# Kernel tuning notes

Hardware: AMD Instinct MI355X
Metric: run time of the kernel (lower is better)

Reference implementation:

```python
import jax, jax.numpy as jnp
import numpy as np
import math

D_MODEL = 1024
MEM_SIZE = 4096
N_HEADS = 8
BATCH = 4
SEQ = 1024
TOP_K = min(SEQ, MEM_SIZE // 10)  # 409, matches torch: min(seq_len, memory_size//10)
UPDATE_RATE = 0.01


def _gelu(x):
    return jax.nn.gelu(x, approximate=False)  # torch nn.GELU default (erf)


def setup_inputs() -> dict:
    key = jax.random.key(0)
    ks = jax.random.split(key, 26)
    w = lambda k, shape, s=0.02: (jax.random.normal(k, shape, jnp.float32) * s)
    inp = {
        "x": jax.random.normal(ks[0], (BATCH, SEQ, D_MODEL), jnp.float32),
        "memory_bank": jax.random.normal(ks[1], (MEM_SIZE, D_MODEL), jnp.float32) * 0.1,
        "memory_indices": jax.random.randint(ks[2], (BATCH, TOP_K), 0, MEM_SIZE, jnp.int32),
        # memory_encoder: Linear -> GELU -> Linear
        "enc_w1": w(ks[3], (D_MODEL, D_MODEL)), "enc_b1": jnp.zeros((D_MODEL,), jnp.float32),
        "enc_w2": w(ks[4], (D_MODEL, D_MODEL)), "enc_b2": jnp.zeros((D_MODEL,), jnp.float32),
        # MultiheadAttention in/out projections
        "wq": w(ks[5], (D_MODEL, D_MODEL)), "bq": jnp.zeros((D_MODEL,), jnp.float32),
        "wk": w(ks[6], (D_MODEL, D_MODEL)), "bk": jnp.zeros((D_MODEL,), jnp.float32),
        "wv": w(ks[7], (D_MODEL, D_MODEL)), "bv": jnp.zeros((D_MODEL,), jnp.float32),
        "wo": w(ks[8], (D_MODEL, D_MODEL)), "bo": jnp.zeros((D_MODEL,), jnp.float32),
        # memory_decoder: Linear -> GELU -> Linear
        "dec_w1": w(ks[9], (D_MODEL, D_MODEL)), "dec_b1": jnp.zeros((D_MODEL,), jnp.float32),
        "dec_w2": w(ks[10], (D_MODEL, D_MODEL)), "dec_b2": jnp.zeros((D_MODEL,), jnp.float32),
        # LayerNorm
        "ln_g": jnp.ones((D_MODEL,), jnp.float32), "ln_b": jnp.zeros((D_MODEL,), jnp.float32),
        # importance_scorer: Linear(d,64) -> GELU -> Linear(64,1) -> Sigmoid
        "imp_w1": w(ks[11], (D_MODEL, 64)), "imp_b1": jnp.zeros((64,), jnp.float32),
        "imp_w2": w(ks[12], (64, 1)), "imp_b2": jnp.zeros((1,), jnp.float32),
    }
    return inp


def reference(x, memory_bank, memory_indices,
              enc_w1, enc_b1, enc_w2, enc_b2,
              wq, bq, wk, bk, wv, bv, wo, bo,
              dec_w1, dec_b1, dec_w2, dec_b2,
              ln_g, ln_b, imp_w1, imp_b1, imp_w2, imp_b2):
    B, L, D = x.shape
    M = memory_bank.shape[0]
    H = N_HEADS
    dh = D // H

    # memory_encoder (dropout inactive at eval)
    enc = _gelu(x @ enc_w1 + enc_b1) @ enc_w2 + enc_b2  # [B,L,D]

    # cross-attention: query = encoded input, key/value = memory bank (shared across batch)
    q = (enc @ wq + bq).reshape(B, L, H, dh)
    k = (memory_bank @ wk + bk).reshape(M, H, dh)
    v = (memory_bank @ wv + bv).reshape(M, H, dh)
    scores = jnp.einsum('blhd,mhd->bhlm', q, k) * (1.0 / math.sqrt(dh))
    attn = jax.nn.softmax(scores, axis=-1)                 # [B,H,L,M]
    ctx = jnp.einsum('bhlm,mhd->blhd', attn, v).reshape(B, L, D)
    mem_out = ctx @ wo + bo

    # memory_decoder + residual + LayerNorm
    dec = _gelu(mem_out @ dec_w1 + dec_b1) @ dec_w2 + dec_b2
    comb = x + dec
    mu = jnp.mean(comb, axis=-1, keepdims=True)
    var = jnp.var(comb, axis=-1, keepdims=True)
    out = (comb - mu) / jnp.sqrt(var + 1e-5) * ln_g + ln_b  # [B,L,D]

    # _update_memory: importance top-k select + sequential EMA scatter into memory bank
    imp = jax.nn.sigmoid(_gelu(x @ imp_w1 + imp_b1) @ imp_w2 + imp_b2)[..., 0]  # [B,L]
    _, top_idx = jax.lax.top_k(imp, TOP_K)                  # [B,K]
    top_tok = jnp.take_along_axis(x, top_idx[..., None], axis=1)  # [B,K,D]

    # faithful to the torch double loop (b outer, k inner): sequential EMA with
    # chained updates on index collisions
    flat_idx = memory_indices.reshape(-1)
    flat_tok = top_tok.reshape(-1, D)

    def body(mem, xs):
        i, t = xs
        row = (1.0 - UPDATE_RATE) * mem[i] + UPDATE_RATE * t
        return mem.at[i].set(row), None

    new_mem, _ = jax.lax.scan(body, memory_bank, (flat_idx, flat_tok))
    return out, new_mem
```

## Files before the change

### kernel.cpp

```cpp
#include <hip/hip_runtime.h>

typedef unsigned short u16;
typedef __attribute__((ext_vector_type(4))) int i4;
typedef __attribute__((ext_vector_type(4))) unsigned u4;
typedef __attribute__((ext_vector_type(4))) unsigned short us4;
typedef __attribute__((ext_vector_type(8))) short short8;
typedef __attribute__((ext_vector_type(4))) float f4;

#define D_MODEL 1024
#define ROWS 4096
#define NHEAD 8
#define DH 128
#define TOPK 409
#define NUPD 1636
#define NBATCH 4
#define MAXC 64
#define ATTNROWS 32768

__device__ __forceinline__ u16 f2bf(float f) {
  unsigned u = __builtin_bit_cast(unsigned, f);
  u += 0x7fffu + ((u >> 16) & 1u);
  return (u16)(u >> 16);
}
__device__ __forceinline__ float bf2f(u16 b) {
  unsigned u = ((unsigned)b) << 16;
  return __builtin_bit_cast(float, u);
}
__device__ __forceinline__ float gelu_f(float v) {
  return 0.5f * v * (1.0f + erff(v * 0.70710678118654752f));
}
__device__ __forceinline__ void gload16(const void* g, void* l) {
  __builtin_amdgcn_global_load_lds((const __attribute__((address_space(1))) void*)g,
                                   (__attribute__((address_space(3))) void*)l, 16, 0, 0);
}

__global__ __launch_bounds__(256) void conv2_kernel(const float* __restrict__ in0,
                                                    u16* __restrict__ out0,
                                                    const float* __restrict__ in1,
                                                    u16* __restrict__ out1, int nb) {
  int bid = blockIdx.x;
  const float* in = (bid < nb) ? in0 : in1;
  u16* out = (bid < nb) ? out0 : out1;
  int i = (bid < nb ? bid : bid - nb) * 256 + threadIdx.x;
  f4 v = ((const f4*)in)[i];
  us4 o;
  o.x = f2bf(v.x); o.y = f2bf(v.y); o.z = f2bf(v.z); o.w = f2bf(v.w);
  ((us4*)out)[i] = o;
}

__global__ __launch_bounds__(256) void wtrans8_kernel(const float* s0, const float* s1,
                                                      const float* s2, const float* s3,
                                                      const float* s4, const float* s5,
                                                      const float* s6, const float* s7,
                                                      u16* __restrict__ dst) {
  const float* srcs[8] = {s0, s1, s2, s3, s4, s5, s6, s7};
  const float* w = srcs[blockIdx.z];
  u16* wt = dst + (size_t)blockIdx.z * (1024 * 1024);
  __shared__ float t[32][33];
  int tx = threadIdx.x & 31, ty = threadIdx.x >> 5;
  int k0 = blockIdx.y * 32, n0 = blockIdx.x * 32;
  for (int r = 0; r < 4; ++r)
    t[ty + r * 8][tx] = w[(size_t)(k0 + ty + r * 8) * 1024 + n0 + tx];
  __syncthreads();
  for (int r = 0; r < 4; ++r)
    wt[(size_t)(n0 + ty + r * 8) * 1024 + k0 + tx] = f2bf(t[tx][ty + r * 8]);
}

__global__ __launch_bounds__(256) void bias_partB(const float* __restrict__ pbuf,
                                                  const float* __restrict__ bq,
                                                  const float* __restrict__ db1,
                                                  float* __restrict__ bqp,
                                                  float* __restrict__ bodp) {
  int id = blockIdx.x;
  int which = id >> 2;
  int n = (id & 3) * 256 + threadIdx.x;
  float s = 0.0f;
  for (int kb = 0; kb < 8; ++kb) s += pbuf[(size_t)(which * 8 + kb) * 1024 + n];
  float* out = which ? bodp : bqp;
  const float* badd = which ? db1 : bq;
  out[n] = s + badd[n];
}

__device__ __forceinline__ void gemm_core(const u16* __restrict__ A,
                                          const u16* __restrict__ BT,
                                          char* al, char* bl, int m0, int n0,
                                          f4 acc[4][2]) {
  const int K = 1024;
  const int tid = threadIdx.x;
  const int lane = tid & 63;
  const int g = lane >> 4, qi = lane & 15;
  const int wid = tid >> 6;
  const int wr = wid >> 1, wc = wid & 1;
  const int a0r = tid >> 2, a0b = (tid & 3) ^ ((a0r >> 1) & 3);
  const int c1 = tid + 256;
  const int a1r = c1 >> 2, a1b = (c1 & 3) ^ ((a1r >> 1) & 3);
  const int b0r = tid >> 2, b0b = (tid & 3) ^ ((b0r >> 1) & 3);

#define STAGE(buf, kt)                                                                   \
  {                                                                                      \
    const int k0_ = (kt) * 32;                                                           \
    gload16(A + (size_t)(m0 + a0r) * K + k0_ + a0b * 8, al + (buf) * 8192 + tid * 16);   \
    gload16(A + (size_t)(m0 + a1r) * K + k0_ + a1b * 8, al + (buf) * 8192 + c1 * 16);    \
    gload16(BT + (size_t)(n0 + b0r) * K + k0_ + b0b * 8, bl + (buf) * 4096 + tid * 16);  \
  }

  STAGE(0, 0);
  __syncthreads();
  int cur = 0;
  for (int kt = 0; kt < 32; ++kt) {
    if (kt + 1 < 32) STAGE(cur ^ 1, kt + 1);
    short8 af[4], bfr[2];
    for (int i = 0; i < 4; ++i) {
      int r = wr * 64 + i * 16 + qi;
      af[i] = *(const short8*)(al + cur * 8192 + r * 64 + ((g ^ ((r >> 1) & 3))) * 16);
    }
    for (int sn = 0; sn < 2; ++sn) {
      int r = wc * 32 + sn * 16 + qi;
      bfr[sn] = *(const short8*)(bl + cur * 4096 + r * 64 + ((g ^ ((r >> 1) & 3))) * 16);
    }
    for (int i = 0; i < 4; ++i)
      for (int sn = 0; sn < 2; ++sn)
        acc[i][sn] = __builtin_amdgcn_mfma_f32_16x16x32_bf16(af[i], bfr[sn], acc[i][sn], 0, 0, 0);
    __syncthreads();
    cur ^= 1;
  }
#undef STAGE
}

__global__ __launch_bounds__(256) void mega_kernel(
    const u16* __restrict__ Akv, const u16* __restrict__ BTkv,
    const float* __restrict__ bk, const float* __restrict__ bv,
    u16* __restrict__ Ck, u16* __restrict__ CvT,
    const u16* __restrict__ Ae, const u16* __restrict__ BTe,
    const float* __restrict__ be, u16* __restrict__ Ce,
    const u16* __restrict__ A0, const u16* __restrict__ B0, u16* __restrict__ C0,
    const u16* __restrict__ A1, const u16* __restrict__ B1, u16* __restrict__ C1,
    const float* __restrict__ b2, const float* __restrict__ wqf,
    const float* __restrict__ bo, const float* __restrict__ dw1,
    float* __restrict__ pbuf) {
  __shared__ __align__(16) char pool[2 * 128 * 64 + 2 * 64 * 64];
  char* al = pool;
  char* bl = pool + 2 * 128 * 64;
  const int gid = blockIdx.x;
  const int tid = threadIdx.x;
  const int lane = tid & 63, wid = tid >> 6;
  const int g = lane >> 4, qi = lane & 15;
  const int wr = wid >> 1, wc = wid & 1;

  if (gid < 1024) {
    const int xcd = gid & 7, j = gid >> 3;
    const int m0 = ((j & 3) * 8 + xcd) * 128;
    const int n0 = (j >> 2) * 64;
    f4 acc[4][2] = {};
    gemm_core(Akv, BTkv, al, bl, m0, n0, acc);
    if (n0 < 1024) {
      for (int i = 0; i < 4; ++i) {
        int row = m0 + wr * 64 + i * 16 + g * 4;
        for (int sn = 0; sn < 2; ++sn) {
          int col = n0 + wc * 32 + sn * 16 + qi;
          float bvv = bk[col];
          for (int jj = 0; jj < 4; ++jj)
            Ck[(size_t)(row + jj) * 1024 + col] = f2bf(acc[i][sn][jj] + bvv);
        }
      }
    } else {
      u16(*t)[132] = (u16(*)[132])pool;
      __syncthreads();
      for (int i = 0; i < 4; ++i)
        for (int sn = 0; sn < 2; ++sn) {
          int nl = wc * 32 + sn * 16 + qi;
          float bvv = bv[n0 - 1024 + nl];
          for (int jj = 0; jj < 4; ++jj)
            t[nl][wr * 64 + i * 16 + g * 4 + jj] = f2bf(acc[i][sn][jj] + bvv);
        }
      __syncthreads();
      int r = tid >> 2, cg = tid & 3;
      for (int v = 0; v < 4; ++v) {
        us4 val = *(const us4*)&t[r][cg * 32 + v * 8];
        *(us4*)&CvT[(size_t)(n0 - 1024 + r) * 4096 + m0 + cg * 32 + v * 8] = val;
      }
    }
  } else if (gid < 1536) {
    const int id = gid - 1024;
    const int xcd = id & 7, j = id >> 3;
    const int m0 = ((j & 3) * 8 + xcd) * 128;
    const int n0 = (j >> 2) * 64;
    f4 acc[4][2] = {};
    gemm_core(Ae, BTe, al, bl, m0, n0, acc);
    for (int i = 0; i < 4; ++i) {
      int row = m0 + wr * 64 + i * 16 + g * 4;
      for (int sn = 0; sn < 2; ++sn) {
        int col = n0 + wc * 32 + sn * 16 + qi;
        float bv = be[col];
        for (int jj = 0; jj < 4; ++jj)
          Ce[(size_t)(row + jj) * 1024 + col] = f2bf(gelu_f(acc[i][sn][jj] + bv));
      }
    }
  } else if (gid < 1792) {
    const int id = gid - 1536;
    const int which = id >> 7, j = id & 127;
    const u16* A = which ? A1 : A0;
    const u16* BT = which ? B1 : B0;
    u16* C = which ? C1 : C0;
    const int m0 = (j >> 4) * 128, n0 = (j & 15) * 64;
    f4 acc[4][2] = {};
    gemm_core(A, BT, al, bl, m0, n0, acc);
    for (int i = 0; i < 4; ++i) {
      int row = m0 + wr * 64 + i * 16 + g * 4;
      for (int sn = 0; sn < 2; ++sn) {
        int col = n0 + wc * 32 + sn * 16 + qi;
        for (int jj = 0; jj < 4; ++jj)
          C[(size_t)(row + jj) * 1024 + col] = f2bf(acc[i][sn][jj]);
      }
    }
  } else {
    const int lid = gid - 1792;
    const int which = lid >> 5;
    const int kb = (lid >> 2) & 7;
    const int n = (lid & 3) * 256 + tid;
    const float* bvec = which ? bo : b2;
    const float* W = which ? dw1 : wqf;
    float s = 0.0f;
    for (int k = kb * 128; k < kb * 128 + 128; ++k) s += bvec[k] * W[(size_t)k * 1024 + n];
    pbuf[(size_t)(which * 8 + kb) * 1024 + n] = s;
  }
}

template <int EPI>
__global__ __launch_bounds__(256) void gemm_bt(const u16* __restrict__ A,
                                               const u16* __restrict__ BT,
                                               const float* __restrict__ bias,
                                               void* __restrict__ C) {
  __shared__ __align__(16) char al[2 * 128 * 64];
  __shared__ __align__(16) char bl[2 * 64 * 64];
  const int N = 1024;
  const int id = blockIdx.x;
  const int xcd = id & 7, j = id >> 3;
  const int m0 = ((j & 3) * 8 + xcd) * 128;
  const int n0 = (j >> 2) * 64;
  const int tid = threadIdx.x;
  const int lane = tid & 63, wid = tid >> 6;
  const int g = lane >> 4, qi = lane & 15;
  const int wr = wid >> 1, wc = wid & 1;
  f4 acc[4][2] = {};
  gemm_core(A, BT, al, bl, m0, n0, acc);
  for (int i = 0; i < 4; ++i) {
    int row = m0 + wr * 64 + i * 16 + g * 4;
    for (int sn = 0; sn < 2; ++sn) {
      int col = n0 + wc * 32 + sn * 16 + qi;
      float bv = bias[col];
      for (int jj = 0; jj < 4; ++jj) {
        float v = acc[i][sn][jj] + bv;
        if constexpr (EPI == 1) v = gelu_f(v);
        if constexpr (EPI == 2)
          ((float*)C)[(size_t)(row + jj) * N + col] = v;
        else
          ((u16*)C)[(size_t)(row + jj) * N + col] = f2bf(v);
      }
    }
  }
}

template <int LP>
__global__ __launch_bounds__(512) void attn_kernel(const u16* __restrict__ q,
                                                   const u16* __restrict__ kp,
                                                   const u16* __restrict__ vT,
                                                   u16* __restrict__ cp0, u16* __restrict__ cp1,
                                                   u16* __restrict__ cp2, u16* __restrict__ cp3,
                                                   float* __restrict__ ml) {
  constexpr int MR = 4096 >> LP;
  constexpr int NT = MR / 64;
  __shared__ __align__(16) char kl[64 * 256];
  __shared__ __align__(16) char vl[128 * 128];
  const int id = blockIdx.x;
  const int h = id & 7;
  const int rest = id >> 3;
  const int part = rest & ((1 << LP) - 1);
  const int qblk = (rest >> LP) & 7;
  const int b = rest >> (3 + LP);
  const int tid = threadIdx.x;
  const int lane = tid & 63, wid = tid >> 6;
  const int g = lane >> 4, qi = lane & 15;
  const int qrow = b * 1024 + qblk * 128 + wid * 16 + qi;
  const float scale = 0.08838834764831845f;
  u16* ctp = (part == 0) ? cp0 : (part == 1) ? cp1 : (part == 2) ? cp2 : cp3;

  short8 qf[4];
  for (int kk = 0; kk < 4; ++kk)
    qf[kk] = *(const short8*)(q + (size_t)qrow * 1024 + h * 128 + kk * 32 + g * 8);

  const int kc0 = tid, kc1 = tid + 512;
  const int kr0 = kc0 >> 4, kb0 = kc0 & 15, kr1 = kc1 >> 4, kb1 = kc1 & 15;
  const int vr0 = kc0 >> 3, vb0 = kc0 & 7, vr1 = kc1 >> 3, vb1 = kc1 & 7;
  const int kd0 = kr0 * 256 + (kb0 ^ (kr0 & 7)) * 16;
  const int kd1 = kr1 * 256 + (kb1 ^ (kr1 & 7)) * 16;
  const int vd0 = vr0 * 128 + (vb0 ^ (vr0 & 7)) * 16;
  const int vd1 = vr1 * 128 + (vb1 ^ (vr1 & 7)) * 16;
  const int mbase = part * MR;
  const u16* kg0 = kp + (size_t)kr0 * 1024 + h * 128 + kb0 * 8;
  const u16* kg1 = kp + (size_t)kr1 * 1024 + h * 128 + kb1 * 8;
  const u16* vg0 = vT + (size_t)(h * 128 + vr0) * 4096 + vb0 * 8;
  const u16* vg1 = vT + (size_t)(h * 128 + vr1) * 4096 + vb1 * 8;

  i4 kreg0, kreg1, vreg0, vreg1;
#define LOADREGS(mt_)                                  \
  {                                                    \
    const int m0_ = mbase + (mt_) * 64;                \
    kreg0 = *(const i4*)(kg0 + (size_t)m0_ * 1024);    \
    kreg1 = *(const i4*)(kg1 + (size_t)m0_ * 1024);    \
    vreg0 = *(const i4*)(vg0 + m0_);                   \
    vreg1 = *(const i4*)(vg1 + m0_);                   \
  }

  f4 ct[8] = {};
  float mrun = -1e30f, lsum = 0.0f;

  LOADREGS(0);
  for (int mt = 0; mt < NT; ++mt) {
    __syncthreads();
    *(i4*)(kl + kd0) = kreg0;
    *(i4*)(kl + kd1) = kreg1;
    *(i4*)(vl + vd0) = vreg0;
    *(i4*)(vl + vd1) = vreg1;
    __syncthreads();
    if (mt + 1 < NT) LOADREGS(mt + 1);

    f4 st[4] = {};
    for (int s = 0; s < 4; ++s) {
      int n = s * 16 + qi;
      const char* krow = kl + n * 256;
      int sw = n & 7;
      for (int kk = 0; kk < 4; ++kk) {
        short8 a = *(const short8*)(krow + ((kk * 4 + g) ^ sw) * 16);
        st[s] = __builtin_amdgcn_mfma_f32_16x16x32_bf16(a, qf[kk], st[s], 0, 0, 0);
      }
    }
    float sv[16];
    float tmax = -1e30f;
    for (int s = 0; s < 4; ++s)
      for (int jj = 0; jj < 4; ++jj) {
        float v = st[s][jj] * scale;
        sv[s * 4 + jj] = v;
        tmax = fmaxf(tmax, v);
      }
    tmax = fmaxf(tmax, __shfl_xor(tmax, 16, 64));
    tmax = fmaxf(tmax, __shfl_xor(tmax, 32, 64));
    float mnew = fmaxf(mrun, tmax);
    float r = __expf(mrun - mnew);
    float psum = 0.0f;
    for (int i = 0; i < 16; ++i) {
      sv[i] = __expf(sv[i] - mnew);
      psum += sv[i];
    }
    psum += __shfl_xor(psum, 16, 64);
    psum += __shfl_xor(psum, 32, 64);
    lsum = lsum * r + psum;
    mrun = mnew;
    for (int i = 0; i < 8; ++i) ct[i] = ct[i] * r;

    unsigned pk0[4], pk1[4];
    for (int s = 0; s < 4; ++s) {
      pk0[s] = (unsigned)f2bf(sv[s * 4 + 0]) | ((unsigned)f2bf(sv[s * 4 + 1]) << 16);
      pk1[s] = (unsigned)f2bf(sv[s * 4 + 2]) | ((unsigned)f2bf(sv[s * 4 + 3]) << 16);
    }
    const int src1 = qi + ((g & 1) << 5);
    const int src2 = src1 + 16;
    const bool hi = (g & 2) != 0;
    for (int p = 0; p < 2; ++p) {
      unsigned a0 = __shfl(pk0[2 * p], src1, 64), b0 = __shfl(pk0[2 * p + 1], src1, 64);
      unsigned a1 = __shfl(pk1[2 * p], src1, 64), b1 = __shfl(pk1[2 * p + 1], src1, 64);
      unsigned a2 = __shfl(pk0[2 * p], src2, 64), b2 = __shfl(pk0[2 * p + 1], src2, 64);
      unsigned a3 = __shfl(pk1[2 * p], src2, 64), b3 = __shfl(pk1[2 * p + 1], src2, 64);
      u4 bw;
      bw.x = hi ? b0 : a0; bw.y = hi ? b1 : a1; bw.z = hi ? b2 : a2; bw.w = hi ? b3 : a3;
      short8 pf = __builtin_bit_cast(short8, bw);
      for (int d = 0; d < 8; ++d) {
        int dr = d * 16 + qi;
        short8 a = *(const short8*)(vl + dr * 128 + (((p * 4 + g) ^ (dr & 7))) * 16);
        ct[d] = __builtin_amdgcn_mfma_f32_16x16x32_bf16(a, pf, ct[d], 0, 0, 0);
      }
    }
  }
#undef LOADREGS

  const int orow = ((b * 8 + h) << 10) + qblk * 128 + wid * 16 + qi;
  if (g == 0) {
    ml[(size_t)(part * ATTNROWS + orow) * 2 + 0] = mrun;
    ml[(size_t)(part * ATTNROWS + orow) * 2 + 1] = lsum;
  }
  for (int d = 0; d < 8; ++d) {
    us4 o;
    o.x = f2bf(ct[d][0]); o.y = f2bf(ct[d][1]);
    o.z = f2bf(ct[d][2]); o.w = f2bf(ct[d][3]);
    *(us4*)(ctp + (size_t)orow * 128 + d * 16 + g * 4) = o;
  }
}

__global__ __launch_bounds__(256) void combine4_kernel(const u16* __restrict__ cp0,
                                                       const u16* __restrict__ cp1,
                                                       const u16* __restrict__ cp2,
                                                       const u16* __restrict__ cp3,
                                                       const float* __restrict__ ml,
                                                       u16* __restrict__ ctx) {
  int tid = threadIdx.x;
  int row = blockIdx.x * 16 + (tid >> 4);
  int dp = (tid & 15) * 8;
  float m0 = ml[(size_t)row * 2], l0 = ml[(size_t)row * 2 + 1];
  float m1 = ml[((size_t)ATTNROWS + row) * 2], l1 = ml[((size_t)ATTNROWS + row) * 2 + 1];
  float m2 = ml[((size_t)2 * ATTNROWS + row) * 2], l2 = ml[((size_t)2 * ATTNROWS + row) * 2 + 1];
  float m3 = ml[((size_t)3 * ATTNROWS + row) * 2], l3 = ml[((size_t)3 * ATTNROWS + row) * 2 + 1];
  float m = fmaxf(fmaxf(m0, m1), fmaxf(m2, m3));
  float s0 = __expf(m0 - m), s1 = __expf(m1 - m), s2 = __expf(m2 - m), s3 = __expf(m3 - m);
  float inv = 1.0f / (l0 * s0 + l1 * s1 + l2 * s2 + l3 * s3);
  short8 c0 = *(const short8*)(cp0 + (size_t)row * 128 + dp);
  short8 c1 = *(const short8*)(cp1 + (size_t)row * 128 + dp);
  short8 c2 = *(const short8*)(cp2 + (size_t)row * 128 + dp);
  short8 c3 = *(const short8*)(cp3 + (size_t)row * 128 + dp);
  us4 o[2];
  for (int i = 0; i < 8; ++i) {
    float f = (bf2f((u16)c0[i]) * s0 + bf2f((u16)c1[i]) * s1 + bf2f((u16)c2[i]) * s2 +
               bf2f((u16)c3[i]) * s3) * inv;
    ((u16*)o)[i] = f2bf(f);
  }
  int bb = row >> 13, hh = (row >> 10) & 7, qr = row & 1023;
  *(short8*)(ctx + (size_t)((bb << 10) + qr) * 1024 + hh * 128 + dp) =
      __builtin_bit_cast(short8, o);
}

__global__ __launch_bounds__(256) void ln_kernel(const float* __restrict__ x,
                                                 const float* __restrict__ dec,
                                                 const float* __restrict__ gw,
                                                 const float* __restrict__ bw,
                                                 float* __restrict__ out,
                                                 int* __restrict__ cnt) {
  __shared__ float rs[256], rs2[256];
  int row = blockIdx.x, tid = threadIdx.x;
  if (tid == 0) cnt[row] = 0;
  float c[4];
  float s = 0.0f, s2 = 0.0f;
  for (int i = 0; i < 4; ++i) {
    int col = tid + i * 256;
    float v = x[(size_t)row * 1024 + col] + dec[(size_t)row * 1024 + col];
    c[i] = v; s += v; s2 += v * v;
  }
  rs[tid] = s; rs2[tid] = s2;
  __syncthreads();
  for (int st = 128; st > 0; st >>= 1) {
    if (tid < st) { rs[tid] += rs[tid + st]; rs2[tid] += rs2[tid + st]; }
    __syncthreads();
  }
  float mu = rs[0] * (1.0f / 1024.0f);
  float var = rs2[0] * (1.0f / 1024.0f) - mu * mu;
  float inv = rsqrtf(var + 1e-5f);
  for (int i = 0; i < 4; ++i) {
    int col = tid + i * 256;
    out[(size_t)row * 1024 + col] = (c[i] - mu) * inv * gw[col] + bw[col];
  }
}

__global__ __launch_bounds__(256) void imp_kernel(const float* __restrict__ x,
                                                  const float* __restrict__ w1,
                                                  const float* __restrict__ b1,
                                                  const float* __restrict__ w2,
                                                  const float* __restrict__ b2,
                                                  float* __restrict__ imp) {
  __shared__ float xs[8][1024];
  int tid = threadIdx.x;
  int lane = tid & 63, wid = tid >> 6;
  size_t base = (size_t)blockIdx.x * 8192;
  for (int i = 0; i < 32; ++i) ((float*)xs)[tid + i * 256] = x[base + tid + i * 256];
  __syncthreads();
  int r0 = wid * 2, r1 = wid * 2 + 1;
  float a0 = 0.0f, a1 = 0.0f;
  for (int k = 0; k < 1024; ++k) {
    float wv = w1[k * 64 + lane];
    a0 += xs[r0][k] * wv;
    a1 += xs[r1][k] * wv;
  }
  float h0 = gelu_f(a0 + b1[lane]) * w2[lane];
  float h1 = gelu_f(a1 + b1[lane]) * w2[lane];
  for (int d = 1; d < 64; d <<= 1) {
    h0 += __shfl_xor(h0, d, 64);
    h1 += __shfl_xor(h1, d, 64);
  }
  if (lane == 0) {
    imp[blockIdx.x * 8 + r0] = 1.0f / (1.0f + expf(-(h0 + b2[0])));
    imp[blockIdx.x * 8 + r1] = 1.0f / (1.0f + expf(-(h1 + b2[0])));
  }
}

__global__ __launch_bounds__(512) void topk_kernel(const float* __restrict__ imp,
                                                   int* __restrict__ tidx) {
  __shared__ float v[1024];
  __shared__ int ix[1024];
  int b = blockIdx.x, tid = threadIdx.x;
  for (int i = tid; i < 1024; i += 512) { v[i] = imp[b * 1024 + i]; ix[i] = i; }
  __syncthreads();
  for (int k = 2; k <= 1024; k <<= 1) {
    for (int j = k >> 1; j > 0; j >>= 1) {
      for (int t = tid; t < 1024; t += 512) {
        int p = t ^ j;
        if (p > t) {
          float va = v[t], vb = v[p];
          int ia = ix[t], ib = ix[p];
          bool ord = (va > vb) || (va == vb && ia < ib);
          bool up = ((t & k) == 0);
          if (up ? !ord : ord) { v[t] = vb; v[p] = va; ix[t] = ib; ix[p] = ia; }
        }
      }
      __syncthreads();
    }
  }
  for (int t = tid; t < TOPK; t += 512) tidx[b * TOPK + t] = ix[t];
}

__global__ __launch_bounds__(128) void rank_kernel(const int* __restrict__ midx,
                                                   int* __restrict__ cnt,
                                                   int* __restrict__ slot) {
  __shared__ int mi[NUPD];
  int tid = threadIdx.x;
  for (int i = tid; i < NUPD; i += 128) mi[i] = midx[i];
  __syncthreads();
  int j = blockIdx.x * 128 + tid;
  if (j < NUPD) {
    int r = mi[j], rank = 0;
    for (int jp = 0; jp < j; ++jp) rank += (mi[jp] == r) ? 1 : 0;
    if (rank < MAXC) slot[r * MAXC + rank] = j;
    atomicAdd(&cnt[r], 1);
  }
}

__global__ __launch_bounds__(256) void apply_kernel(const float* __restrict__ x,
                                                    const float* __restrict__ mem,
                                                    const int* __restrict__ tidx,
                                                    const int* __restrict__ cnt,
                                                    const int* __restrict__ slot,
                                                    float* __restrict__ outm) {
  int row = blockIdx.x, tid = threadIdx.x;
  f4 acc = ((const f4*)(mem + (size_t)row * 1024))[tid];
  int c = cnt[row];
  c = c < MAXC ? c : MAXC;
  for (int t = 0; t < c; ++t) {
    int j = slot[row * MAXC + t];
    int b = j / TOPK;
    int tr = tidx[j];
    f4 xv = ((const f4*)(x + ((size_t)b * 1024 + tr) * 1024))[tid];
    acc = acc * 0.99f + xv * 0.01f;
  }
  ((f4*)(outm + (size_t)row * 1024))[tid] = acc;
}

extern "C" void kernel_launch(void* const* d_in, const int* in_sizes, int n_in,
                              void* d_out, int out_size, void* d_ws, size_t ws_size,
                              hipStream_t stream) {
  const float* x = (const float*)d_in[0];
  const float* memory_bank = (const float*)d_in[1];
  const int* memory_indices = (const int*)d_in[2];
  const float* enc_w1 = (const float*)d_in[3];
  const float* enc_b1 = (const float*)d_in[4];
  const float* enc_w2 = (const float*)d_in[5];
  const float* enc_b2 = (const float*)d_in[6];
  const float* wq = (const float*)d_in[7];
  const float* bq = (const float*)d_in[8];
  const float* wk = (const float*)d_in[9];
  const float* bk = (const float*)d_in[10];
  const float* wv = (const float*)d_in[11];
  const float* bv = (const float*)d_in[12];
  const float* wo = (const float*)d_in[13];
  const float* bo = (const float*)d_in[14];
  const float* dec_w1 = (const float*)d_in[15];
  const float* dec_b1 = (const float*)d_in[16];
  const float* dec_w2 = (const float*)d_in[17];
  const float* dec_b2 = (const float*)d_in[18];
  const float* ln_g = (const float*)d_in[19];
  const float* ln_b = (const float*)d_in[20];
  const float* imp_w1 = (const float*)d_in[21];
  const float* imp_b1 = (const float*)d_in[22];
  const float* imp_w2 = (const float*)d_in[23];
  const float* imp_b2 = (const float*)d_in[24];

  char* ws = (char*)d_ws;
  u16* buf0 = (u16*)(ws);
  u16* buf1 = (u16*)(ws + (8ull << 20));
  u16* buf2 = (u16*)(ws + (16ull << 20));
  u16* buf3 = (u16*)(ws + (24ull << 20));
  u16* buf4 = (u16*)(ws + (32ull << 20));
  float* decb = (float*)(ws + (40ull << 20));
  u16* wtb = (u16*)(ws + (56ull << 20));
  float* impb = (float*)(ws + (72ull << 20));
  int* tidx = (int*)(ws + (72ull << 20) + (1 << 16));
  float* bqp = (float*)(ws + (72ull << 20) + (1 << 17));
  float* bodp = (float*)(ws + (72ull << 20) + (1 << 17) + 4096);
  float* pbuf = (float*)(ws + (72ull << 20) + 196608);
  int* cnt = (int*)buf3;
  int* slot = (int*)(ws + (24ull << 20) + (1 << 16));
  u16* w2n = (u16*)(ws + (40ull << 20));
  u16* won = (u16*)(ws + (42ull << 20));
  u16* cp0 = buf1;
  u16* cp1 = buf2;
  u16* cp2 = (u16*)(ws + (40ull << 20));
  u16* cp3 = (u16*)(ws + (48ull << 20));
  float* ml = (float*)(ws + (56ull << 20));

  const int NM = 1024 * 1024;
  u16* wt_e1 = wtb + 0 * NM;
  u16* wt_e2q = wtb + 1 * NM;
  u16* wt_q = wtb + 2 * NM;
  u16* wt_k = wtb + 3 * NM;
  u16* wt_od = wtb + 5 * NM;
  u16* wt_d1 = wtb + 6 * NM;
  u16* wt_d2 = wtb + 7 * NM;

  conv2_kernel<<<8192, 256, 0, stream>>>(x, buf0, memory_bank, buf2, 4096);
  wtrans8_kernel<<<dim3(32, 32, 8), 256, 0, stream>>>(enc_w1, enc_w2, wq, wk, wv, wo,
                                                      dec_w1, dec_w2, wtb);
  conv2_kernel<<<2048, 256, 0, stream>>>(enc_w2, w2n, wo, won, 1024);

  mega_kernel<<<1856, 256, 0, stream>>>(buf2, wt_k, bk, bv, buf3, buf4,
                                        buf0, wt_e1, enc_b1, buf1,
                                        wt_q, w2n, wt_e2q, wt_d1, won, wt_od,
                                        enc_b2, wq, bo, dec_w1, pbuf);
  bias_partB<<<8, 256, 0, stream>>>(pbuf, bq, dec_b1, bqp, bodp);

  gemm_bt<0><<<512, 256, 0, stream>>>(buf1, wt_e2q, bqp, buf0);

  attn_kernel<2><<<1024, 512, 0, stream>>>(buf0, buf3, buf4, cp0, cp1, cp2, cp3, ml);
  combine4_kernel<<<2048, 256, 0, stream>>>(cp0, cp1, cp2, cp3, ml, buf0);

  gemm_bt<1><<<512, 256, 0, stream>>>(buf0, wt_od, bodp, buf1);
  gemm_bt<2><<<512, 256, 0, stream>>>(buf1, wt_d2, dec_b2, decb);
  ln_kernel<<<4096, 256, 0, stream>>>(x, decb, ln_g, ln_b, (float*)d_out, cnt);

  imp_kernel<<<512, 256, 0, stream>>>(x, imp_w1, imp_b1, imp_w2, imp_b2, impb);
  topk_kernel<<<NBATCH, 512, 0, stream>>>(impb, tidx);
  rank_kernel<<<13, 128, 0, stream>>>(memory_indices, cnt, slot);
  apply_kernel<<<4096, 256, 0, stream>>>(x, memory_bank, tidx, cnt, slot,
                                         (float*)d_out + (size_t)ROWS * D_MODEL);
}
```

Before: 398.8 us.

## Fold importance scorer into mega kernel and use exp2 lazy-rescale softmax in attention

Moves the importance-scorer MLP into extra blocks of the mega kernel, removing one launch and letting it overlap with the GEMM blocks. The shared pool grows to 32KB so it can hold the x rows. Q is now prescaled by the softmax scale times log2(e) in the Q-projection epilogue, and attention uses exp2. The running max is only rescaled when the new tile max exceeds it by more than 8, cutting per-tile rescale work at the cost of looser bounds on the exponent range. Larger LDS per block may lower occupancy for the GEMM blocks in the mega kernel.

```diff
diff --git a/kernel.cpp b/kernel.cpp
--- a/kernel.cpp
+++ b/kernel.cpp
@@ -16,6 +16,7 @@
 #define NBATCH 4
 #define MAXC 64
 #define ATTNROWS 32768
+#define QSCALE 0.1275174038f
 
 __device__ __forceinline__ u16 f2bf(float f) {
   unsigned u = __builtin_bit_cast(unsigned, f);
@@ -137,8 +138,11 @@
     const u16* __restrict__ A1, const u16* __restrict__ B1, u16* __restrict__ C1,
     const float* __restrict__ b2, const float* __restrict__ wqf,
     const float* __restrict__ bo, const float* __restrict__ dw1,
-    float* __restrict__ pbuf) {
-  __shared__ __align__(16) char pool[2 * 128 * 64 + 2 * 64 * 64];
+    float* __restrict__ pbuf,
+    const float* __restrict__ x, const float* __restrict__ iw1,
+    const float* __restrict__ ib1, const float* __restrict__ iw2,
+    const float* __restrict__ ib2, float* __restrict__ imp) {
+  __shared__ __align__(16) char pool[32768];
   char* al = pool;
   char* bl = pool + 2 * 128 * 64;
   const int gid = blockIdx.x;
@@ -213,7 +217,7 @@
           C[(size_t)(row + jj) * 1024 + col] = f2bf(acc[i][sn][jj]);
       }
     }
-  } else {
+  } else if (gid < 1856) {
     const int lid = gid - 1792;
     const int which = lid >> 5;
     const int kb = (lid >> 2) & 7;
@@ -223,6 +227,29 @@
     float s = 0.0f;
     for (int k = kb * 128; k < kb * 128 + 128; ++k) s += bvec[k] * W[(size_t)k * 1024 + n];
     pbuf[(size_t)(which * 8 + kb) * 1024 + n] = s;
+  } else {
+    const int lid = gid - 1856;
+    float* xs = (float*)pool;
+    size_t base = (size_t)lid * 8192;
+    for (int i = 0; i < 32; ++i) xs[tid + i * 256] = x[base + tid + i * 256];
+    __syncthreads();
+    int r0 = wid * 2, r1 = wid * 2 + 1;
+    float a0 = 0.0f, a1 = 0.0f;
+    for (int k = 0; k < 1024; ++k) {
+      float wv = iw1[k * 64 + lane];
+      a0 += xs[r0 * 1024 + k] * wv;
+      a1 += xs[r1 * 1024 + k] * wv;
+    }
+    float h0 = gelu_f(a0 + ib1[lane]) * iw2[lane];
+    float h1 = gelu_f(a1 + ib1[lane]) * iw2[lane];
+    for (int d = 1; d < 64; d <<= 1) {
+      h0 += __shfl_xor(h0, d, 64);
+      h1 += __shfl_xor(h1, d, 64);
+    }
+    if (lane == 0) {
+      imp[lid * 8 + r0] = 1.0f / (1.0f + expf(-(h0 + ib2[0])));
+      imp[lid * 8 + r1] = 1.0f / (1.0f + expf(-(h1 + ib2[0])));
+    }
   }
 }
 
@@ -252,6 +279,7 @@
       for (int jj = 0; jj < 4; ++jj) {
         float v = acc[i][sn][jj] + bv;
         if constexpr (EPI == 1) v = gelu_f(v);
+        if constexpr (EPI == 4) v = v * QSCALE;
         if constexpr (EPI == 2)
           ((float*)C)[(size_t)(row + jj) * N + col] = v;
         else
@@ -282,7 +310,6 @@
   const int lane = tid & 63, wid = tid >> 6;
   const int g = lane >> 4, qi = lane & 15;
   const int qrow = b * 1024 + qblk * 128 + wid * 16 + qi;
-  const float scale = 0.08838834764831845f;
   u16* ctp = (part == 0) ? cp0 : (part == 1) ? cp1 : (part == 2) ? cp2 : cp3;
 
   short8 qf[4];
@@ -336,27 +363,30 @@
       }
     }
     float sv[16];
-    float tmax = -1e30f;
+    float tm = -1e30f;
     for (int s = 0; s < 4; ++s)
       for (int jj = 0; jj < 4; ++jj) {
-        float v = st[s][jj] * scale;
-        sv[s * 4 + jj] = v;
-        tmax = fmaxf(tmax, v);
-      }
-    tmax = fmaxf(tmax, __shfl_xor(tmax, 16, 64));
-    tmax = fmaxf(tmax, __shfl_xor(tmax, 32, 64));
-    float mnew = fmaxf(mrun, tmax);
-    float r = __expf(mrun - mnew);
+        sv[s * 4 + jj] = st[s][jj];
+        tm = fmaxf(tm, st[s][jj]);
+      }
+    tm = fmaxf(tm, __shfl_xor(tm, 16, 64));
+    tm = fmaxf(tm, __shfl_xor(tm, 32, 64));
+    if (!__all(tm <= mrun + 8.0f)) {
+      float mnew = fmaxf(mrun, tm);
+      float r = exp2f(mrun - mnew);
+      lsum *= r;
+      for (int i = 0; i < 8; ++i) ct[i] = ct[i] * r;
+      mrun = mnew;
+    }
     float psum = 0.0f;
     for (int i = 0; i < 16; ++i) {
-      sv[i] = __expf(sv[i] - mnew);
-      psum += sv[i];
+      float p = exp2f(sv[i] - mrun);
+      sv[i] = p;
+      psum += p;
     }
     psum += __shfl_xor(psum, 16, 64);
     psum += __shfl_xor(psum, 32, 64);
-    lsum = lsum * r + psum;
-    mrun = mnew;
-    for (int i = 0; i < 8; ++i) ct[i] = ct[i] * r;
+    lsum += psum;
 
     unsigned pk0[4], pk1[4];
     for (int s = 0; s < 4; ++s) {
@@ -410,7 +440,7 @@
   float m2 = ml[((size_t)2 * ATTNROWS + row) * 2], l2 = ml[((size_t)2 * ATTNROWS + row) * 2 + 1];
   float m3 = ml[((size_t)3 * ATTNROWS + row) * 2], l3 = ml[((size_t)3 * ATTNROWS + row) * 2 + 1];
   float m = fmaxf(fmaxf(m0, m1), fmaxf(m2, m3));
-  float s0 = __expf(m0 - m), s1 = __expf(m1 - m), s2 = __expf(m2 - m), s3 = __expf(m3 - m);
+  float s0 = exp2f(m0 - m), s1 = exp2f(m1 - m), s2 = exp2f(m2 - m), s3 = exp2f(m3 - m);
   float inv = 1.0f / (l0 * s0 + l1 * s1 + l2 * s2 + l3 * s3);
   short8 c0 = *(const short8*)(cp0 + (size_t)row * 128 + dp);
   short8 c1 = *(const short8*)(cp1 + (size_t)row * 128 + dp);
@@ -455,37 +485,6 @@
   for (int i = 0; i < 4; ++i) {
     int col = tid + i * 256;
     out[(size_t)row * 1024 + col] = (c[i] - mu) * inv * gw[col] + bw[col];
-  }
-}
-
-__global__ __launch_bounds__(256) void imp_kernel(const float* __restrict__ x,
-                                                  const float* __restrict__ w1,
-                                                  const float* __restrict__ b1,
-                                                  const float* __restrict__ w2,
-                                                  const float* __restrict__ b2,
-                                                  float* __restrict__ imp) {
-  __shared__ float xs[8][1024];
-  int tid = threadIdx.x;
-  int lane = tid & 63, wid = tid >> 6;
-  size_t base = (size_t)blockIdx.x * 8192;
-  for (int i = 0; i < 32; ++i) ((float*)xs)[tid + i * 256] = x[base + tid + i * 256];
-  __syncthreads();
-  int r0 = wid * 2, r1 = wid * 2 + 1;
-  float a0 = 0.0f, a1 = 0.0f;
-  for (int k = 0; k < 1024; ++k) {
-    float wv = w1[k * 64 + lane];
-    a0 += xs[r0][k] * wv;
-    a1 += xs[r1][k] * wv;
-  }
-  float h0 = gelu_f(a0 + b1[lane]) * w2[lane];
-  float h1 = gelu_f(a1 + b1[lane]) * w2[lane];
-  for (int d = 1; d < 64; d <<= 1) {
-    h0 += __shfl_xor(h0, d, 64);
-    h1 += __shfl_xor(h1, d, 64);
-  }
-  if (lane == 0) {
-    imp[blockIdx.x * 8 + r0] = 1.0f / (1.0f + expf(-(h0 + b2[0])));
-    imp[blockIdx.x * 8 + r1] = 1.0f / (1.0f + expf(-(h1 + b2[0])));
   }
 }
 
@@ -616,13 +615,14 @@
                                                       dec_w1, dec_w2, wtb);
   conv2_kernel<<<2048, 256, 0, stream>>>(enc_w2, w2n, wo, won, 1024);
 
-  mega_kernel<<<1856, 256, 0, stream>>>(buf2, wt_k, bk, bv, buf3, buf4,
+  mega_kernel<<<2368, 256, 0, stream>>>(buf2, wt_k, bk, bv, buf3, buf4,
                                         buf0, wt_e1, enc_b1, buf1,
                                         wt_q, w2n, wt_e2q, wt_d1, won, wt_od,
-                                        enc_b2, wq, bo, dec_w1, pbuf);
+                                        enc_b2, wq, bo, dec_w1, pbuf,
+                                        x, imp_w1, imp_b1, imp_w2, imp_b2, impb);
   bias_partB<<<8, 256, 0, stream>>>(pbuf, bq, dec_b1, bqp, bodp);
 
-  gemm_bt<0><<<512, 256, 0, stream>>>(buf1, wt_e2q, bqp, buf0);
+  gemm_bt<4><<<512, 256, 0, stream>>>(buf1, wt_e2q, bqp, buf0);
 
   attn_kernel<2><<<1024, 512, 0, stream>>>(buf0, buf3, buf4, cp0, cp1, cp2, cp3, ml);
   combine4_kernel<<<2048, 256, 0, stream>>>(cp0, cp1, cp2, cp3, ml, buf0);
@@ -631,7 +631,6 @@
   gemm_bt<2><<<512, 256, 0, stream>>>(buf1, wt_d2, dec_b2, decb);
   ln_kernel<<<4096, 256, 0, stream>>>(x, decb, ln_g, ln_b, (float*)d_out, cnt);
 
-  imp_kernel<<<512, 256, 0, stream>>>(x, imp_w1, imp_b1, imp_w2, imp_b2, impb);
   topk_kernel<<<NBATCH, 512, 0, stream>>>(impb, tidx);
   rank_kernel<<<13, 128, 0, stream>>>(memory_indices, cnt, slot);
   apply_kernel<<<4096, 256, 0, stream>>>(x, memory_bank, tidx, cnt, slot,
```

New measurement: 394.6 us. About the same (-1.0%).
